# Kernel tuning notes

Hardware: AMD Instinct MI355X
Metric: run time of the kernel (lower is better)

The kernel has to match this reference:

```python
import jax, jax.numpy as jnp
import numpy as np

ORG_VOCAB = 32000
EXTRA = 256
MAX_LORAS = 8
RANK = 16
D = 2048
B, S = 2, 2048


def setup_inputs() -> dict:
    key = jax.random.key(0)
    k1, k2, k3, k4, k5 = jax.random.split(key, 5)
    x = jax.random.randint(k1, (B, S), 0, ORG_VOCAB + EXTRA, dtype=jnp.int64 if jax.config.jax_enable_x64 else jnp.int32)
    lora_indices = jax.random.randint(k2, (B * S,), 0, MAX_LORAS, dtype=x.dtype)
    base_weight = jax.random.normal(k3, (ORG_VOCAB + MAX_LORAS * EXTRA, D), dtype=jnp.float32)
    lora_a_stacked = jax.random.normal(k4, (MAX_LORAS, ORG_VOCAB + EXTRA, RANK), dtype=jnp.float32) * 0.02
    lora_b_stacked = jax.random.normal(k5, (MAX_LORAS, D, RANK), dtype=jnp.float32) * 0.02
    return {"x": x, "lora_indices": lora_indices, "base_weight": base_weight,
            "lora_a_stacked": lora_a_stacked, "lora_b_stacked": lora_b_stacked}


def reference(x, lora_indices, base_weight, lora_a_stacked, lora_b_stacked):
    xf = x.reshape(-1)                      # [T] token ids
    li = lora_indices                       # [T] per-token lora index
    added = xf >= ORG_VOCAB                 # added_tokens_mask
    # LoRA A gather: row = lora_idx*(org_vocab+extra) + token_id (embeddings_indices[1])
    a2d = lora_a_stacked.reshape(-1, RANK)  # [max_loras*(org+extra), r]
    a = a2d[li * (ORG_VOCAB + EXTRA) + xf]  # [T, r]
    # Base embedding: added tokens offset by lora_idx*extra (embeddings_indices[0])
    base_idx = xf + jnp.where(added, li * EXTRA, 0)
    full_output = base_weight[base_idx]     # [T, D]
    # bgmv combine: out[t] += lora_b[li[t]] @ a[t]
    b = lora_b_stacked[li]                  # [T, D, r]
    out = full_output + jnp.einsum('tr,tdr->td', a, b)
    return out.reshape(x.shape + (D,))
```

## Files before the change

### kernel.cpp

```cpp
#include <hip/hip_runtime.h>


constexpr int ORG_VOCAB = 32000;
constexpr int EXTRA     = 256;
constexpr int RANK      = 16;
constexpr int D         = 2048;
constexpr int NLORA     = 8;
constexpr int SPLIT     = 32;
constexpr int SLEN      = 128;
constexpr int DCHUNK    = 512;
constexpr int NY        = D / DCHUNK;
constexpr int BLK       = 256;

__global__ __launch_bounds__(BLK, 4) void lora_fused_k(
    const int*   __restrict__ x,
    const int*   __restrict__ li,
    const float* __restrict__ base_w,
    const float* __restrict__ lora_a,
    const float* __restrict__ lora_b,
    float*       __restrict__ out,
    int T)
{
    const int l      = blockIdx.x >> 5;
    const int stripe = blockIdx.x & (SPLIT - 1);
    const int y      = blockIdx.y;
    const int tid    = threadIdx.x;
    const int t0     = stripe * SLEN;

    __shared__ float sb[DCHUNK][RANK + 1];
    __shared__ int   s_tok[SLEN], s_bidx[SLEN], s_li[SLEN];
    __shared__ int   s_mt[SLEN];
    __shared__ int   s_nm;
    __shared__ float s_ab[2][8][RANK];

    const float* __restrict__ bsrc =
        lora_b + ((size_t)l * D + (size_t)y * DCHUNK) * RANK;
    #pragma unroll
    for (int k = 0; k < (DCHUNK * RANK) / (BLK * 4); ++k) {
        const int g4 = k * BLK + tid;
        const float4 v = ((const float4*)bsrc)[g4];
        const int d  = g4 >> 2;
        const int r4 = (g4 & 3) * 4;
        sb[d][r4 + 0] = v.x; sb[d][r4 + 1] = v.y;
        sb[d][r4 + 2] = v.z; sb[d][r4 + 3] = v.w;
    }

    if (tid < SLEN) {
        const int t = t0 + tid;
        int lt = -1, tok = 0;
        if (t < T) { lt = li[t]; tok = x[t]; }
        s_li[tid]   = lt;
        s_tok[tid]  = tok;
        s_bidx[tid] = tok + (tok >= ORG_VOCAB ? lt * EXTRA : 0);
    }
    __syncthreads();

    if (tid < 64) {
        const unsigned long long below = (tid == 63) ? 0x7fffffffffffffffull
                                                     : ((1ull << tid) - 1ull);
        const bool f0 = (s_li[tid] == l);
        const unsigned long long m0 = __ballot(f0);
        const bool f1 = (s_li[tid + 64] == l);
        const unsigned long long m1 = __ballot(f1);
        const int c0 = __popcll(m0);
        if (f0) s_mt[__popcll(m0 & below)] = tid;
        if (f1) s_mt[c0 + __popcll(m1 & below)] = tid + 64;
        if (tid == 0) s_nm = c0 + __popcll(m1);
    }

    float bt0[RANK], bt1[RANK];
    __syncthreads();
    #pragma unroll
    for (int r = 0; r < RANK; ++r) {
        bt0[r] = sb[tid][r];
        bt1[r] = sb[tid + 256][r];
    }

    const int nm = s_nm;
    const size_t d0 = (size_t)y * DCHUNK + tid;

    int par = 0;
    for (int mb = 0; mb < nm; mb += 8, par ^= 1) {
        const int nb = (nm - mb < 8) ? (nm - mb) : 8;

        {
            const int i = tid >> 4, r = tid & 15;
            if (tid < 128 && i < nb) {
                const int k = s_mt[mb + i];
                s_ab[par][i][r] =
                    lora_a[((size_t)l * (ORG_VOCAB + EXTRA) + (size_t)s_tok[k]) * RANK + r];
            }
        }

        float b0[8], b1[8];
        #pragma unroll
        for (int i = 0; i < 8; ++i) {
            const int ii = (i < nb) ? i : (nb - 1);
            const int k  = s_mt[mb + ii];
            const float* __restrict__ br = base_w + (size_t)s_bidx[k] * D + d0;
            b0[i] = br[0];
            b1[i] = br[256];
        }

        __syncthreads();

        #pragma unroll
        for (int i = 0; i < 8; ++i) {
            if (i >= nb) break;
            const int k = s_mt[mb + i];
            const float4 a0 = *(const float4*)&s_ab[par][i][0];
            const float4 a1 = *(const float4*)&s_ab[par][i][4];
            const float4 a2 = *(const float4*)&s_ab[par][i][8];
            const float4 a3 = *(const float4*)&s_ab[par][i][12];
            float acc0 = b0[i], acc1 = b1[i];
            acc0 += a0.x*bt0[0]  + a0.y*bt0[1]  + a0.z*bt0[2]  + a0.w*bt0[3]
                  + a1.x*bt0[4]  + a1.y*bt0[5]  + a1.z*bt0[6]  + a1.w*bt0[7]
                  + a2.x*bt0[8]  + a2.y*bt0[9]  + a2.z*bt0[10] + a2.w*bt0[11]
                  + a3.x*bt0[12] + a3.y*bt0[13] + a3.z*bt0[14] + a3.w*bt0[15];
            acc1 += a0.x*bt1[0]  + a0.y*bt1[1]  + a0.z*bt1[2]  + a0.w*bt1[3]
                  + a1.x*bt1[4]  + a1.y*bt1[5]  + a1.z*bt1[6]  + a1.w*bt1[7]
                  + a2.x*bt1[8]  + a2.y*bt1[9]  + a2.z*bt1[10] + a2.w*bt1[11]
                  + a3.x*bt1[12] + a3.y*bt1[13] + a3.z*bt1[14] + a3.w*bt1[15];
            const int t = t0 + k;
            float* __restrict__ orow = out + (size_t)t * D + d0;
            orow[0]   = acc0;
            orow[256] = acc1;
        }
    }
}

extern "C" void kernel_launch(void* const* d_in, const int* in_sizes, int n_in,
                              void* d_out, int out_size, void* d_ws, size_t ws_size,
                              hipStream_t stream) {
    const int*   x      = (const int*)d_in[0];
    const int*   li     = (const int*)d_in[1];
    const float* base_w = (const float*)d_in[2];
    const float* lora_a = (const float*)d_in[3];
    const float* lora_b = (const float*)d_in[4];
    float*       out    = (float*)d_out;

    int T = in_sizes[0];

    dim3 grid(NLORA * SPLIT, NY);
    lora_fused_k<<<grid, BLK, 0, stream>>>(x, li, base_w, lora_a, lora_b, out, T);
}
```

Before: 21.35 us.

## Double-buffer base-row gathers, use float2 accesses, and halve token stripe length

Halves the token stripe to 64 so one wavefront ballot builds the per-LoRA token list, doubling the grid. Each thread now owns two adjacent output columns and uses float2 loads and stores. The LoRA A rows for all matched tokens are staged into shared memory once, and the per-batch barrier is removed. Base-weight gathers are double-buffered so the next batch's loads are issued while the current batch is computed and stored. Blocks with no matching tokens exit early, but the B tile load is repeated across twice as many blocks, and the extra buffers add register pressure.

After: 20.97 us. Within noise of the previous version (-1.8%).

```diff
diff --git a/kernel.cpp b/kernel.cpp
--- a/kernel.cpp
+++ b/kernel.cpp
@@ -6,11 +6,51 @@
 constexpr int RANK      = 16;
 constexpr int D         = 2048;
 constexpr int NLORA     = 8;
-constexpr int SPLIT     = 32;
-constexpr int SLEN      = 128;
+constexpr int SPLIT     = 64;
+constexpr int SLEN      = 64;
 constexpr int DCHUNK    = 512;
 constexpr int NY        = D / DCHUNK;
 constexpr int BLK       = 256;
+
+__device__ __forceinline__ void load_batch(
+    float2* buf, int mb, int nm,
+    const int* s_mt, const int* s_bidx,
+    const float* __restrict__ base_w, int d0)
+{
+    #pragma unroll
+    for (int i = 0; i < 8; ++i) {
+        const int ii = (mb + i < nm) ? (mb + i) : (nm - 1);
+        const int k  = s_mt[ii];
+        buf[i] = *(const float2*)(base_w + (size_t)s_bidx[k] * D + d0);
+    }
+}
+
+__device__ __forceinline__ void proc_batch(
+    const float2* buf, int mb, int nm, int t0,
+    const int* s_mt, const float (*s_a)[RANK],
+    const float* bt0, const float* bt1,
+    float* __restrict__ out, int d0)
+{
+    #pragma unroll
+    for (int i = 0; i < 8; ++i) {
+        if (mb + i >= nm) break;
+        const int k  = s_mt[mb + i];
+        const float4 a0 = *(const float4*)&s_a[mb + i][0];
+        const float4 a1 = *(const float4*)&s_a[mb + i][4];
+        const float4 a2 = *(const float4*)&s_a[mb + i][8];
+        const float4 a3 = *(const float4*)&s_a[mb + i][12];
+        float2 acc = buf[i];
+        acc.x += a0.x*bt0[0]  + a0.y*bt0[1]  + a0.z*bt0[2]  + a0.w*bt0[3]
+               + a1.x*bt0[4]  + a1.y*bt0[5]  + a1.z*bt0[6]  + a1.w*bt0[7]
+               + a2.x*bt0[8]  + a2.y*bt0[9]  + a2.z*bt0[10] + a2.w*bt0[11]
+               + a3.x*bt0[12] + a3.y*bt0[13] + a3.z*bt0[14] + a3.w*bt0[15];
+        acc.y += a0.x*bt1[0]  + a0.y*bt1[1]  + a0.z*bt1[2]  + a0.w*bt1[3]
+               + a1.x*bt1[4]  + a1.y*bt1[5]  + a1.z*bt1[6]  + a1.w*bt1[7]
+               + a2.x*bt1[8]  + a2.y*bt1[9]  + a2.z*bt1[10] + a2.w*bt1[11]
+               + a3.x*bt1[12] + a3.y*bt1[13] + a3.z*bt1[14] + a3.w*bt1[15];
+        *(float2*)(out + (size_t)(t0 + k) * D + d0) = acc;
+    }
+}
 
 __global__ __launch_bounds__(BLK, 4) void lora_fused_k(
     const int*   __restrict__ x,
@@ -21,17 +61,16 @@
     float*       __restrict__ out,
     int T)
 {
-    const int l      = blockIdx.x >> 5;
+    const int l      = blockIdx.x >> 6;
     const int stripe = blockIdx.x & (SPLIT - 1);
     const int y      = blockIdx.y;
     const int tid    = threadIdx.x;
     const int t0     = stripe * SLEN;
 
     __shared__ float sb[DCHUNK][RANK + 1];
-    __shared__ int   s_tok[SLEN], s_bidx[SLEN], s_li[SLEN];
-    __shared__ int   s_mt[SLEN];
+    __shared__ int   s_tok[SLEN], s_bidx[SLEN], s_mt[SLEN];
     __shared__ int   s_nm;
-    __shared__ float s_ab[2][8][RANK];
+    __shared__ float s_a[SLEN][RANK];
 
     const float* __restrict__ bsrc =
         lora_b + ((size_t)l * D + (size_t)y * DCHUNK) * RANK;
@@ -46,86 +85,50 @@
     }
 
     if (tid < SLEN) {
-        const int t = t0 + tid;
-        int lt = -1, tok = 0;
-        if (t < T) { lt = li[t]; tok = x[t]; }
-        s_li[tid]   = lt;
+        const int t   = t0 + tid;
+        const int lt  = (t < T) ? li[t] : -1;
+        const int tok = (t < T) ? x[t] : 0;
         s_tok[tid]  = tok;
         s_bidx[tid] = tok + (tok >= ORG_VOCAB ? lt * EXTRA : 0);
+        const bool f = (lt == l);
+        const unsigned long long m = __ballot(f);
+        const unsigned long long below = (1ull << tid) - 1ull;
+        if (f) s_mt[__popcll(m & below)] = tid;
+        if (tid == 0) s_nm = __popcll(m);
     }
     __syncthreads();
 
-    if (tid < 64) {
-        const unsigned long long below = (tid == 63) ? 0x7fffffffffffffffull
-                                                     : ((1ull << tid) - 1ull);
-        const bool f0 = (s_li[tid] == l);
-        const unsigned long long m0 = __ballot(f0);
-        const bool f1 = (s_li[tid + 64] == l);
-        const unsigned long long m1 = __ballot(f1);
-        const int c0 = __popcll(m0);
-        if (f0) s_mt[__popcll(m0 & below)] = tid;
-        if (f1) s_mt[c0 + __popcll(m1 & below)] = tid + 64;
-        if (tid == 0) s_nm = c0 + __popcll(m1);
+    const int nm = s_nm;
+    if (nm == 0) return;
+
+    float bt0[RANK], bt1[RANK];
+    #pragma unroll
+    for (int r = 0; r < RANK; ++r) {
+        bt0[r] = sb[2 * tid][r];
+        bt1[r] = sb[2 * tid + 1][r];
     }
 
-    float bt0[RANK], bt1[RANK];
+    for (int j = tid; j < nm * RANK; j += BLK) {
+        const int i = j >> 4, r = j & 15;
+        s_a[i][r] = lora_a[((size_t)l * (ORG_VOCAB + EXTRA)
+                            + (size_t)s_tok[s_mt[i]]) * RANK + r];
+    }
     __syncthreads();
-    #pragma unroll
-    for (int r = 0; r < RANK; ++r) {
-        bt0[r] = sb[tid][r];
-        bt1[r] = sb[tid + 256][r];
-    }
 
-    const int nm = s_nm;
-    const size_t d0 = (size_t)y * DCHUNK + tid;
+    const int d0 = y * DCHUNK + tid * 2;
+    float2 bufA[8], bufB[8];
 
-    int par = 0;
-    for (int mb = 0; mb < nm; mb += 8, par ^= 1) {
-        const int nb = (nm - mb < 8) ? (nm - mb) : 8;
-
-        {
-            const int i = tid >> 4, r = tid & 15;
-            if (tid < 128 && i < nb) {
-                const int k = s_mt[mb + i];
-                s_ab[par][i][r] =
-                    lora_a[((size_t)l * (ORG_VOCAB + EXTRA) + (size_t)s_tok[k]) * RANK + r];
-            }
-        }
-
-        float b0[8], b1[8];
-        #pragma unroll
-        for (int i = 0; i < 8; ++i) {
-            const int ii = (i < nb) ? i : (nb - 1);
-            const int k  = s_mt[mb + ii];
-            const float* __restrict__ br = base_w + (size_t)s_bidx[k] * D + d0;
-            b0[i] = br[0];
-            b1[i] = br[256];
-        }
-
-        __syncthreads();
-
-        #pragma unroll
-        for (int i = 0; i < 8; ++i) {
-            if (i >= nb) break;
-            const int k = s_mt[mb + i];
-            const float4 a0 = *(const float4*)&s_ab[par][i][0];
-            const float4 a1 = *(const float4*)&s_ab[par][i][4];
-            const float4 a2 = *(const float4*)&s_ab[par][i][8];
-            const float4 a3 = *(const float4*)&s_ab[par][i][12];
-            float acc0 = b0[i], acc1 = b1[i];
-            acc0 += a0.x*bt0[0]  + a0.y*bt0[1]  + a0.z*bt0[2]  + a0.w*bt0[3]
-                  + a1.x*bt0[4]  + a1.y*bt0[5]  + a1.z*bt0[6]  + a1.w*bt0[7]
-                  + a2.x*bt0[8]  + a2.y*bt0[9]  + a2.z*bt0[10] + a2.w*bt0[11]
-                  + a3.x*bt0[12] + a3.y*bt0[13] + a3.z*bt0[14] + a3.w*bt0[15];
-            acc1 += a0.x*bt1[0]  + a0.y*bt1[1]  + a0.z*bt1[2]  + a0.w*bt1[3]
-                  + a1.x*bt1[4]  + a1.y*bt1[5]  + a1.z*bt1[6]  + a1.w*bt1[7]
-                  + a2.x*bt1[8]  + a2.y*bt1[9]  + a2.z*bt1[10] + a2.w*bt1[11]
-                  + a3.x*bt1[12] + a3.y*bt1[13] + a3.z*bt1[14] + a3.w*bt1[15];
-            const int t = t0 + k;
-            float* __restrict__ orow = out + (size_t)t * D + d0;
-            orow[0]   = acc0;
-            orow[256] = acc1;
-        }
+    load_batch(bufA, 0, nm, s_mt, s_bidx, base_w, d0);
+    int mb = 0;
+    while (true) {
+        if (mb + 8 < nm) load_batch(bufB, mb + 8, nm, s_mt, s_bidx, base_w, d0);
+        proc_batch(bufA, mb, nm, t0, s_mt, s_a, bt0, bt1, out, d0);
+        mb += 8;
+        if (mb >= nm) break;
+        if (mb + 8 < nm) load_batch(bufA, mb + 8, nm, s_mt, s_bidx, base_w, d0);
+        proc_batch(bufB, mb, nm, t0, s_mt, s_a, bt0, bt1, out, d0);
+        mb += 8;
+        if (mb >= nm) break;
     }
 }
 
```
